# Performance work log

Measured on AMD Instinct MI355X. Metric: run time of the kernel, lower is better.

The kernel has to match this reference:

```python
import jax, jax.numpy as jnp
import numpy as np

D_MODEL = 1024
N_HEADS = 16
D_HEAD = D_MODEL // N_HEADS
WINDOW = 128
D_FF = 3 * D_MODEL
EPS = 1e-5


def _layer_norm(x, g, b):
    mu = jnp.mean(x, axis=-1, keepdims=True)
    var = jnp.var(x, axis=-1, keepdims=True)
    return (x - mu) * jax.lax.rsqrt(var + EPS) * g + b


def setup_inputs() -> dict:
    key = jax.random.key(0)
    ks = jax.random.split(key, 10)
    B, S = 2, 2048
    sd = 0.02
    return {
        "x": jax.random.normal(ks[0], (B, S, D_MODEL), dtype=jnp.float32),
        "w_qkv": jax.random.normal(ks[1], (D_MODEL, 3 * D_MODEL), dtype=jnp.float32) * sd,
        "b_qkv": jnp.zeros((3 * D_MODEL,), jnp.float32),
        "w_out": jax.random.normal(ks[2], (D_MODEL, D_MODEL), dtype=jnp.float32) * sd,
        "b_out": jnp.zeros((D_MODEL,), jnp.float32),
        "w_ff1": jax.random.normal(ks[3], (D_MODEL, D_FF), dtype=jnp.float32) * sd,
        "b_ff1": jnp.zeros((D_FF,), jnp.float32),
        "w_ff2": jax.random.normal(ks[4], (D_FF, D_MODEL), dtype=jnp.float32) * sd,
        "b_ff2": jnp.zeros((D_MODEL,), jnp.float32),
        "ln1_g": jnp.ones((D_MODEL,), jnp.float32),
        "ln1_b": jnp.zeros((D_MODEL,), jnp.float32),
        "ln2_g": jnp.ones((D_MODEL,), jnp.float32),
        "ln2_b": jnp.zeros((D_MODEL,), jnp.float32),
    }


def reference(x, w_qkv, b_qkv, w_out, b_out, w_ff1, b_ff1, w_ff2, b_ff2,
              ln1_g, ln1_b, ln2_g, ln2_b):
    B, S, D = x.shape
    h = _layer_norm(x, ln1_g, ln1_b)
    qkv = (h @ w_qkv + b_qkv).reshape(B, S, 3, N_HEADS, D_HEAD)
    q, k, v = (jnp.moveaxis(qkv[:, :, i], 1, 2) for i in range(3))  # (B,H,S,dh)
    scores = jnp.einsum('bhqd,bhkd->bhqk', q, k) / jnp.sqrt(jnp.float32(D_HEAD))
    i = jnp.arange(S)[:, None]
    j = jnp.arange(S)[None, :]
    allowed = (j <= i) & (j > i - WINDOW)  # causal sliding window band
    scores = jnp.where(allowed, scores, -jnp.inf)
    attn = jax.nn.softmax(scores, axis=-1)
    ctx = jnp.einsum('bhqk,bhkd->bqhd', attn, v).reshape(B, S, D)
    x = x + (ctx @ w_out + b_out)
    h2 = _layer_norm(x, ln2_g, ln2_b)
    ff = jax.nn.gelu(h2 @ w_ff1 + b_ff1, approximate=False) @ w_ff2 + b_ff2
    return x + ff
```

## Files before the change

kernel.cpp:

```cpp
#include <hip/hip_runtime.h>

#define D_MODEL 1024
#define SEQ 2048
#define BATCH 2
#define NH 16
#define DH 64
#define WIN 128
#define DFF 3072

typedef __bf16 bf16x8 __attribute__((ext_vector_type(8)));
typedef float f32x4 __attribute__((ext_vector_type(4)));
typedef unsigned short u16;
typedef unsigned int u32;

__device__ __forceinline__ float b2f(u16 u) {
    unsigned int x = ((unsigned int)u) << 16;
    return __uint_as_float(x);
}
__device__ __forceinline__ u16 f2b(float f) {
    unsigned int x = __float_as_uint(f);
    x += 0x7fffu + ((x >> 16) & 1u);
    return (u16)(x >> 16);
}
__device__ __forceinline__ u32 pk2(float a, float b) {
    return (u32)f2b(a) | ((u32)f2b(b) << 16);
}

#define WAIT_VMCNT0() __builtin_amdgcn_s_waitcnt(0x0F70)

__global__ __launch_bounds__(256) void prep_k(
        const float* __restrict__ x, const float* __restrict__ g1,
        const float* __restrict__ bt1, u16* __restrict__ hbf,
        const float* __restrict__ wqkv, u16* __restrict__ wqkvT,
        const float* __restrict__ wout, u16* __restrict__ woutT,
        const float* __restrict__ wff1, u16* __restrict__ wff1T,
        const float* __restrict__ wff2, u16* __restrict__ wff2T) {
    __shared__ u16 tile[32][33];
    __shared__ float s1[4], s2[4];
    int bid = blockIdx.x;
    if (bid < 10240) {
        const float* in; u16* out; int R, C, loc, gx;
        if (bid < 3072)      { in = wqkv; out = wqkvT; R = 1024; C = 3072; loc = bid;        gx = 96; }
        else if (bid < 4096) { in = wout; out = woutT; R = 1024; C = 1024; loc = bid - 3072; gx = 32; }
        else if (bid < 7168) { in = wff1; out = wff1T; R = 1024; C = 3072; loc = bid - 4096; gx = 96; }
        else                 { in = wff2; out = wff2T; R = 3072; C = 1024; loc = bid - 7168; gx = 32; }
        int bx = loc % gx, by = loc / gx;
        int tx = threadIdx.x & 31, ty = threadIdx.x >> 5;
        int r0 = by * 32, c0 = bx * 32;
#pragma unroll
        for (int i = 0; i < 4; ++i)
            tile[ty + i * 8][tx] = f2b(in[(size_t)(r0 + ty + i * 8) * C + c0 + tx]);
        __syncthreads();
#pragma unroll
        for (int i = 0; i < 4; ++i)
            out[(size_t)(c0 + ty + i * 8) * R + r0 + tx] = tile[tx][ty + i * 8];
    } else {
        int row = bid - 10240;
        const float* xr = x + (size_t)row * D_MODEL;
        float v[4];
        float sum = 0.f, sq = 0.f;
#pragma unroll
        for (int i = 0; i < 4; ++i) {
            v[i] = xr[threadIdx.x + i * 256];
            sum += v[i];
            sq += v[i] * v[i];
        }
#pragma unroll
        for (int off = 32; off > 0; off >>= 1) {
            sum += __shfl_xor(sum, off, 64);
            sq  += __shfl_xor(sq, off, 64);
        }
        int w = threadIdx.x >> 6;
        if ((threadIdx.x & 63) == 0) { s1[w] = sum; s2[w] = sq; }
        __syncthreads();
        sum = s1[0] + s1[1] + s1[2] + s1[3];
        sq  = s2[0] + s2[1] + s2[2] + s2[3];
        float mu = sum * (1.f / D_MODEL);
        float var = sq * (1.f / D_MODEL) - mu * mu;
        float rstd = rsqrtf(var + 1e-5f);
        u16* outr = hbf + (size_t)row * D_MODEL;
#pragma unroll
        for (int i = 0; i < 4; ++i) {
            int c = threadIdx.x + i * 256;
            outr[c] = f2b((v[i] - mu) * rstd * g1[c] + bt1[c]);
        }
    }
}

__global__ __launch_bounds__(256) void ln_k(
        const float* __restrict__ x, const float* __restrict__ g,
        const float* __restrict__ bta, u16* __restrict__ out) {
    int row = blockIdx.x;
    const float* xr = x + (size_t)row * D_MODEL;
    float v[4];
    float sum = 0.f, sq = 0.f;
#pragma unroll
    for (int i = 0; i < 4; ++i) {
        v[i] = xr[threadIdx.x + i * 256];
        sum += v[i];
        sq += v[i] * v[i];
    }
#pragma unroll
    for (int off = 32; off > 0; off >>= 1) {
        sum += __shfl_xor(sum, off, 64);
        sq  += __shfl_xor(sq, off, 64);
    }
    __shared__ float s1[4], s2[4];
    int w = threadIdx.x >> 6;
    if ((threadIdx.x & 63) == 0) { s1[w] = sum; s2[w] = sq; }
    __syncthreads();
    sum = s1[0] + s1[1] + s1[2] + s1[3];
    sq  = s2[0] + s2[1] + s2[2] + s2[3];
    float mu = sum * (1.f / D_MODEL);
    float var = sq * (1.f / D_MODEL) - mu * mu;
    float rstd = rsqrtf(var + 1e-5f);
    u16* outr = out + (size_t)row * D_MODEL;
#pragma unroll
    for (int i = 0; i < 4; ++i) {
        int c = threadIdx.x + i * 256;
        outr[c] = f2b((v[i] - mu) * rstd * g[c] + bta[c]);
    }
}

template <int GELU, int VSPLIT>
__global__ __launch_bounds__(256, 3) void gemm3_k(
        const u16* __restrict__ A, const u16* __restrict__ Bt,
        const float* __restrict__ bias, u16* __restrict__ Cb,
        u16* __restrict__ vt, int M, int N, int K, int ldc) {
    __shared__ u16 As[2 * 128 * 64];
    __shared__ u16 Bs[2 * 64 * 64];
    int tid = threadIdx.x;
    int w = tid >> 6, lane = tid & 63;
    int qd = lane >> 4, l15 = lane & 15;

    int lin = blockIdx.x;
    int xcd = lin & 7, idx = lin >> 3;
    int m0 = (xcd * 4 + (idx & 3)) * 128;
    int n0 = (idx >> 2) * 64;

    const u16* gsrc[6];
    u16* ldst[6];
    int nboff[6];
#pragma unroll
    for (int i = 0; i < 6; ++i) {
        int c = w * 6 + i;
        int isA = c < 16;
        int cb = isA ? c : c - 16;
        int row = cb * 8 + (lane >> 3);
        int cg = (lane & 7) ^ (row & 7);
        gsrc[i] = (isA ? A + (size_t)(m0 + row) * K
                       : Bt + (size_t)(n0 + row) * K) + cg * 8;
        ldst[i] = (isA ? As : Bs) + cb * 512;
        nboff[i] = isA ? 8192 : 4096;
    }

    int wm = w & 1, wn = w >> 1;
    f32x4 acc[4][2];
#pragma unroll
    for (int mt = 0; mt < 4; ++mt)
#pragma unroll
        for (int nt = 0; nt < 2; ++nt)
            acc[mt][nt] = (f32x4){0.f, 0.f, 0.f, 0.f};

    int aoff[4][2], boff[2][2];
#pragma unroll
    for (int t = 0; t < 4; ++t) {
        int ar = wm * 64 + t * 16 + l15;
#pragma unroll
        for (int h = 0; h < 2; ++h)
            aoff[t][h] = ar * 64 + (((h * 4 + qd) ^ (ar & 7)) * 8);
    }
#pragma unroll
    for (int t = 0; t < 2; ++t) {
        int br = wn * 32 + t * 16 + l15;
#pragma unroll
        for (int h = 0; h < 2; ++h)
            boff[t][h] = br * 64 + (((h * 4 + qd) ^ (br & 7)) * 8);
    }

#pragma unroll
    for (int i = 0; i < 6; ++i)
        __builtin_amdgcn_global_load_lds(
            (__attribute__((address_space(1))) void*)(gsrc[i]),
            (__attribute__((address_space(3))) void*)(ldst[i]), 16, 0, 0);

    int nsteps = K >> 6;

#define TSTEP3(S, RB)                                                       \
    {                                                                       \
        WAIT_VMCNT0();                                                      \
        __builtin_amdgcn_s_barrier();                                       \
        if ((S) + 1 < nsteps) {                                             \
            int k0 = ((S) + 1) << 6;                                        \
            _Pragma("unroll")                                               \
            for (int i = 0; i < 6; ++i)                                     \
                __builtin_amdgcn_global_load_lds(                           \
                    (__attribute__((address_space(1))) void*)(gsrc[i] + k0),\
                    (__attribute__((address_space(3))) void*)(ldst[i] +     \
                        (1 - (RB)) * nboff[i]),                             \
                    16, 0, 0);                                              \
        }                                                                   \
        bf16x8 av[4][2], bv[2][2];                                          \
        _Pragma("unroll")                                                   \
        for (int t = 0; t < 4; ++t)                                         \
            _Pragma("unroll")                                               \
            for (int h = 0; h < 2; ++h)                                     \
                av[t][h] = *(const bf16x8*)&As[aoff[t][h] + (RB) * 8192];   \
        _Pragma("unroll")                                                   \
        for (int t = 0; t < 2; ++t)                                         \
            _Pragma("unroll")                                               \
            for (int h = 0; h < 2; ++h)                                     \
                bv[t][h] = *(const bf16x8*)&Bs[boff[t][h] + (RB) * 4096];   \
        _Pragma("unroll")                                                   \
        for (int mt = 0; mt < 4; ++mt)                                      \
            _Pragma("unroll")                                               \
            for (int nt = 0; nt < 2; ++nt) {                                \
                acc[mt][nt] = __builtin_amdgcn_mfma_f32_16x16x32_bf16(      \
                    av[mt][0], bv[nt][0], acc[mt][nt], 0, 0, 0);            \
                acc[mt][nt] = __builtin_amdgcn_mfma_f32_16x16x32_bf16(      \
                    av[mt][1], bv[nt][1], acc[mt][nt], 0, 0, 0);            \
            }                                                               \
    }

    for (int s = 0; s < nsteps; s += 2) {
        TSTEP3(s, 0);
        TSTEP3(s + 1, 1);
    }

#pragma unroll
    for (int mt = 0; mt < 4; ++mt) {
        int row0 = m0 + wm * 64 + mt * 16 + qd * 4;
#pragma unroll
        for (int nt = 0; nt < 2; ++nt) {
            int col = n0 + wn * 32 + nt * 16 + l15;
            float v[4];
#pragma unroll
            for (int reg = 0; reg < 4; ++reg) {
                v[reg] = acc[mt][nt][reg] + bias[col];
                if (GELU) v[reg] = 0.5f * v[reg] * (1.f + erff(v[reg] * 0.70710678118654752f));
            }
            if (VSPLIT && col >= 2 * D_MODEL) {
                int d = col - 2 * D_MODEL;
                int bh = (row0 >> 11) * NH + (d >> 6);
                ushort4 pkv = {f2b(v[0]), f2b(v[1]), f2b(v[2]), f2b(v[3])};
                *(ushort4*)&vt[((size_t)(bh * DH + (d & 63))) * SEQ + (row0 & (SEQ - 1))] = pkv;
            } else {
#pragma unroll
                for (int reg = 0; reg < 4; ++reg)
                    Cb[(size_t)(row0 + reg) * ldc + col] = f2b(v[reg]);
            }
        }
    }
}

__global__ __launch_bounds__(256, 3) void gemm_tall_k(
        const u16* __restrict__ A, const u16* __restrict__ Bt,
        const float* __restrict__ bias, const float* __restrict__ resid,
        float* __restrict__ C, int M, int N, int K, int ldc) {
    __shared__ u16 As[2 * 64 * 64];
    __shared__ u16 Bs[2 * 128 * 64];
    int tid = threadIdx.x;
    int w = tid >> 6, lane = tid & 63;
    int qd = lane >> 4, l15 = lane & 15;

    int lin = blockIdx.x;
    int xcd = lin & 7, idx = lin >> 3;
    int m0 = (xcd * 8 + (idx & 7)) * 64;
    int n0 = (idx >> 3) * 128;

    const u16* gsrc[6];
    u16* ldst[6];
    int nboff[6];
#pragma unroll
    for (int i = 0; i < 6; ++i) {
        int c = w * 6 + i;
        int isA = c < 8;
        int cb = isA ? c : c - 8;
        int row = cb * 8 + (lane >> 3);
        int cg = (lane & 7) ^ (row & 7);
        gsrc[i] = (isA ? A + (size_t)(m0 + row) * K
                       : Bt + (size_t)(n0 + row) * K) + cg * 8;
        ldst[i] = (isA ? As : Bs) + cb * 512;
        nboff[i] = isA ? 4096 : 8192;
    }

    int wm = w & 1, wn = w >> 1;
    f32x4 acc[2][4];
#pragma unroll
    for (int mt = 0; mt < 2; ++mt)
#pragma unroll
        for (int nt = 0; nt < 4; ++nt)
            acc[mt][nt] = (f32x4){0.f, 0.f, 0.f, 0.f};

    int aoff[2][2], boff[4][2];
#pragma unroll
    for (int t = 0; t < 2; ++t) {
        int ar = wm * 32 + t * 16 + l15;
#pragma unroll
        for (int h = 0; h < 2; ++h)
            aoff[t][h] = ar * 64 + (((h * 4 + qd) ^ (ar & 7)) * 8);
    }
#pragma unroll
    for (int t = 0; t < 4; ++t) {
        int br = wn * 64 + t * 16 + l15;
#pragma unroll
        for (int h = 0; h < 2; ++h)
            boff[t][h] = br * 64 + (((h * 4 + qd) ^ (br & 7)) * 8);
    }

#pragma unroll
    for (int i = 0; i < 6; ++i)
        __builtin_amdgcn_global_load_lds(
            (__attribute__((address_space(1))) void*)(gsrc[i]),
            (__attribute__((address_space(3))) void*)(ldst[i]), 16, 0, 0);

    int nsteps = K >> 6;

#define TSTEP64(S, RB)                                                      \
    {                                                                       \
        WAIT_VMCNT0();                                                      \
        __builtin_amdgcn_s_barrier();                                       \
        if ((S) + 1 < nsteps) {                                             \
            int k0 = ((S) + 1) << 6;                                        \
            _Pragma("unroll")                                               \
            for (int i = 0; i < 6; ++i)                                     \
                __builtin_amdgcn_global_load_lds(                           \
                    (__attribute__((address_space(1))) void*)(gsrc[i] + k0),\
                    (__attribute__((address_space(3))) void*)(ldst[i] +     \
                        (1 - (RB)) * nboff[i]),                             \
                    16, 0, 0);                                              \
        }                                                                   \
        bf16x8 av[2][2], bv[4][2];                                          \
        _Pragma("unroll")                                                   \
        for (int t = 0; t < 2; ++t)                                         \
            _Pragma("unroll")                                               \
            for (int h = 0; h < 2; ++h)                                     \
                av[t][h] = *(const bf16x8*)&As[aoff[t][h] + (RB) * 4096];   \
        _Pragma("unroll")                                                   \
        for (int t = 0; t < 4; ++t)                                         \
            _Pragma("unroll")                                               \
            for (int h = 0; h < 2; ++h)                                     \
                bv[t][h] = *(const bf16x8*)&Bs[boff[t][h] + (RB) * 8192];   \
        _Pragma("unroll")                                                   \
        for (int mt = 0; mt < 2; ++mt)                                      \
            _Pragma("unroll")                                               \
            for (int nt = 0; nt < 4; ++nt) {                                \
                acc[mt][nt] = __builtin_amdgcn_mfma_f32_16x16x32_bf16(      \
                    av[mt][0], bv[nt][0], acc[mt][nt], 0, 0, 0);            \
                acc[mt][nt] = __builtin_amdgcn_mfma_f32_16x16x32_bf16(      \
                    av[mt][1], bv[nt][1], acc[mt][nt], 0, 0, 0);            \
            }                                                               \
    }

    for (int s = 0; s < nsteps; s += 2) {
        TSTEP64(s, 0);
        TSTEP64(s + 1, 1);
    }

#pragma unroll
    for (int mt = 0; mt < 2; ++mt) {
        int row0 = m0 + wm * 32 + mt * 16 + qd * 4;
#pragma unroll
        for (int nt = 0; nt < 4; ++nt) {
            int col = n0 + wn * 64 + nt * 16 + l15;
#pragma unroll
            for (int reg = 0; reg < 4; ++reg) {
                float v = acc[mt][nt][reg] + bias[col]
                        + resid[(size_t)(row0 + reg) * ldc + col];
                C[(size_t)(row0 + reg) * ldc + col] = v;
            }
        }
    }
}

__global__ __launch_bounds__(256) void attn_k(
        const u16* __restrict__ qk, const u16* __restrict__ vt,
        u16* __restrict__ ctx) {
    int lane = threadIdx.x & 63, l15 = lane & 15, quad = lane >> 4;
    int t = blockIdx.x * 4 + (threadIdx.x >> 6);
    int qt = t & (SEQ / 16 - 1);
    int h  = (t >> 7) & (NH - 1);
    int b  = t >> 11;
    int q0 = qt * 16;
    int bh = b * NH + h;

    const u16* qrow = qk + (size_t)(b * SEQ + q0 + l15) * (2 * D_MODEL) + h * DH + quad * 8;
    bf16x8 qf0 = *(const bf16x8*)(qrow);
    bf16x8 qf1 = *(const bf16x8*)(qrow + 32);
    const u16* kbase = qk + (size_t)(b * SEQ) * (2 * D_MODEL) + D_MODEL + h * DH + quad * 8;
    const u16* vbase = vt + (size_t)(bh * DH) * SEQ;

    f32x4 o[4] = {{0.f, 0.f, 0.f, 0.f}, {0.f, 0.f, 0.f, 0.f},
                  {0.f, 0.f, 0.f, 0.f}, {0.f, 0.f, 0.f, 0.f}};
    float m = -1e30f, l = 0.f;
    int q = q0 + l15;
    int cs = q0 - (WIN - 1);
    cs = cs < 0 ? 0 : (cs & ~31);

    for (int c = cs; c <= q0 + 15; c += 32) {
        const u16* k0p = kbase + (size_t)(c + l15) * (2 * D_MODEL);
        const u16* k1p = k0p + (size_t)16 * (2 * D_MODEL);
        bf16x8 ka0 = *(const bf16x8*)(k0p);
        bf16x8 ka1 = *(const bf16x8*)(k0p + 32);
        bf16x8 kb0 = *(const bf16x8*)(k1p);
        bf16x8 kb1 = *(const bf16x8*)(k1p + 32);
        f32x4 s0 = {0.f, 0.f, 0.f, 0.f}, s1 = {0.f, 0.f, 0.f, 0.f};
        s0 = __builtin_amdgcn_mfma_f32_16x16x32_bf16(ka0, qf0, s0, 0, 0, 0);
        s0 = __builtin_amdgcn_mfma_f32_16x16x32_bf16(ka1, qf1, s0, 0, 0, 0);
        s1 = __builtin_amdgcn_mfma_f32_16x16x32_bf16(kb0, qf0, s1, 0, 0, 0);
        s1 = __builtin_amdgcn_mfma_f32_16x16x32_bf16(kb1, qf1, s1, 0, 0, 0);

        float p0[4], p1[4];
        float cm = -1e30f;
#pragma unroll
        for (int reg = 0; reg < 4; ++reg) {
            int k0i = c + quad * 4 + reg;
            p0[reg] = ((unsigned)(q - k0i) < WIN) ? s0[reg] * 0.125f : -1e30f;
            p1[reg] = ((unsigned)(q - k0i - 16) < WIN) ? s1[reg] * 0.125f : -1e30f;
            cm = fmaxf(cm, fmaxf(p0[reg], p1[reg]));
        }
        cm = fmaxf(cm, __shfl_xor(cm, 16, 64));
        cm = fmaxf(cm, __shfl_xor(cm, 32, 64));
        float mn = fmaxf(m, cm);
        float alpha = __expf(m - mn);
        m = mn;
        float ls = 0.f;
#pragma unroll
        for (int reg = 0; reg < 4; ++reg) {
            p0[reg] = __expf(p0[reg] - mn);
            p1[reg] = __expf(p1[reg] - mn);
            ls += p0[reg] + p1[reg];
        }
        ls += __shfl_xor(ls, 16, 64);
        ls += __shfl_xor(ls, 32, 64);
        l = l * alpha + ls;
#pragma unroll
        for (int mt = 0; mt < 4; ++mt) o[mt] *= alpha;

        u32 z0 = pk2(p0[0], p0[1]), z1 = pk2(p0[2], p0[3]);
        u32 w0 = pk2(p1[0], p1[1]), w1 = pk2(p1[2], p1[3]);
        int slo = ((quad & 1) * 2) * 16 + l15;
        int shi = slo + 16;
        u32 zl0 = (u32)__shfl((int)z0, slo, 64), zl1 = (u32)__shfl((int)z1, slo, 64);
        u32 zh0 = (u32)__shfl((int)z0, shi, 64), zh1 = (u32)__shfl((int)z1, shi, 64);
        u32 wl0 = (u32)__shfl((int)w0, slo, 64), wl1 = (u32)__shfl((int)w1, slo, 64);
        u32 wh0 = (u32)__shfl((int)w0, shi, 64), wh1 = (u32)__shfl((int)w1, shi, 64);
        alignas(16) u32 pr[4];
        pr[0] = quad < 2 ? zl0 : wl0;
        pr[1] = quad < 2 ? zl1 : wl1;
        pr[2] = quad < 2 ? zh0 : wh0;
        pr[3] = quad < 2 ? zh1 : wh1;
        bf16x8 pf = *(const bf16x8*)pr;

#pragma unroll
        for (int mt = 0; mt < 4; ++mt) {
            bf16x8 vf = *(const bf16x8*)(vbase + (size_t)(mt * 16 + l15) * SEQ + c + quad * 8);
            o[mt] = __builtin_amdgcn_mfma_f32_16x16x32_bf16(vf, pf, o[mt], 0, 0, 0);
        }
    }

    float rdiv = 1.f / l;
    u16* crow = ctx + (size_t)(b * SEQ + q0 + l15) * D_MODEL + h * DH;
#pragma unroll
    for (int mt = 0; mt < 4; ++mt) {
        ushort4 pkv = {f2b(o[mt][0] * rdiv), f2b(o[mt][1] * rdiv),
                       f2b(o[mt][2] * rdiv), f2b(o[mt][3] * rdiv)};
        *(ushort4*)(crow + mt * 16 + quad * 4) = pkv;
    }
}

extern "C" void kernel_launch(void* const* d_in, const int* in_sizes, int n_in,
                              void* d_out, int out_size, void* d_ws, size_t ws_size,
                              hipStream_t stream) {
    (void)in_sizes; (void)n_in; (void)out_size; (void)ws_size;
    const float* x     = (const float*)d_in[0];
    const float* w_qkv = (const float*)d_in[1];
    const float* b_qkv = (const float*)d_in[2];
    const float* w_out = (const float*)d_in[3];
    const float* b_out = (const float*)d_in[4];
    const float* w_ff1 = (const float*)d_in[5];
    const float* b_ff1 = (const float*)d_in[6];
    const float* w_ff2 = (const float*)d_in[7];
    const float* b_ff2 = (const float*)d_in[8];
    const float* ln1g  = (const float*)d_in[9];
    const float* ln1b  = (const float*)d_in[10];
    const float* ln2g  = (const float*)d_in[11];
    const float* ln2b  = (const float*)d_in[12];
    float* out = (float*)d_out;

    const int M = BATCH * SEQ;
    char* base = (char*)d_ws;
    u16*   hbf   = (u16*)(base);
    u16*   qkbuf = (u16*)(base + (8ll  << 20));
    u16*   ctxbf = (u16*)(base + (24ll << 20));
    u16*   vtbuf = (u16*)(base + (32ll << 20));
    u16*   ffbf  = (u16*)(base + (8ll  << 20));
    float* x2    = (float*)(base + (40ll << 20));
    u16*   wqkvT = (u16*)(base + (56ll << 20));
    u16*   woutT = (u16*)(base + (62ll << 20));
    u16*   wff1T = (u16*)(base + (64ll << 20));
    u16*   wff2T = (u16*)(base + (70ll << 20));

    prep_k<<<dim3(14336), 256, 0, stream>>>(
        x, ln1g, ln1b, hbf, w_qkv, wqkvT, w_out, woutT,
        w_ff1, wff1T, w_ff2, wff2T);
    gemm3_k<0, 1><<<dim3((M / 128) * (3 * D_MODEL / 64)), 256, 0, stream>>>(
        hbf, wqkvT, b_qkv, qkbuf, vtbuf, M, 3 * D_MODEL, D_MODEL, 2 * D_MODEL);
    attn_k<<<dim3(BATCH * NH * (SEQ / 16) / 4), 256, 0, stream>>>(qkbuf, vtbuf, ctxbf);
    gemm_tall_k<<<dim3(512), 256, 0, stream>>>(
        ctxbf, woutT, b_out, x, x2, M, D_MODEL, D_MODEL, D_MODEL);
    ln_k<<<M, 256, 0, stream>>>(x2, ln2g, ln2b, hbf);
    gemm3_k<1, 0><<<dim3((M / 128) * (DFF / 64)), 256, 0, stream>>>(
        hbf, wff1T, b_ff1, ffbf, nullptr, M, DFF, D_MODEL, DFF);
    gemm_tall_k<<<dim3(512), 256, 0, stream>>>(
        ffbf, wff2T, b_ff2, x2, out, M, D_MODEL, DFF, D_MODEL);
}
```

Measured before the change: 273.1 us.

## Triple-buffer GEMM LDS tiles with two-stage-ahead async prefetch

Changes the GEMM main loop from double to triple buffering in LDS. Loads for step s+2 are issued while step s computes, and the wait uses a partial vmcnt so one stage of loads stays in flight. This is meant to hide global-to-LDS latency better. It costs more LDS per block (occupancy hint drops from 3 to 2 blocks per CU) and adds runtime buffer-index arithmetic in place of the unrolled two-step macro.

```diff
diff --git a/kernel.cpp b/kernel.cpp
--- a/kernel.cpp
+++ b/kernel.cpp
@@ -27,6 +27,7 @@
 }
 
 #define WAIT_VMCNT0() __builtin_amdgcn_s_waitcnt(0x0F70)
+#define WAIT_VMCNT6() __builtin_amdgcn_s_waitcnt(0x0F76)
 
 __global__ __launch_bounds__(256) void prep_k(
         const float* __restrict__ x, const float* __restrict__ g1,
@@ -123,12 +124,12 @@
 }
 
 template <int GELU, int VSPLIT>
-__global__ __launch_bounds__(256, 3) void gemm3_k(
+__global__ __launch_bounds__(256, 2) void gemm3_k(
         const u16* __restrict__ A, const u16* __restrict__ Bt,
         const float* __restrict__ bias, u16* __restrict__ Cb,
         u16* __restrict__ vt, int M, int N, int K, int ldc) {
-    __shared__ u16 As[2 * 128 * 64];
-    __shared__ u16 Bs[2 * 64 * 64];
+    __shared__ u16 As[3 * 128 * 64];
+    __shared__ u16 Bs[3 * 64 * 64];
     int tid = threadIdx.x;
     int w = tid >> 6, lane = tid & 63;
     int qd = lane >> 4, l15 = lane & 15;
@@ -140,7 +141,7 @@
 
     const u16* gsrc[6];
     u16* ldst[6];
-    int nboff[6];
+    int shr[6];
 #pragma unroll
     for (int i = 0; i < 6; ++i) {
         int c = w * 6 + i;
@@ -151,7 +152,7 @@
         gsrc[i] = (isA ? A + (size_t)(m0 + row) * K
                        : Bt + (size_t)(n0 + row) * K) + cg * 8;
         ldst[i] = (isA ? As : Bs) + cb * 512;
-        nboff[i] = isA ? 8192 : 4096;
+        shr[i] = isA ? 0 : 1;
     }
 
     int wm = w & 1, wn = w >> 1;
@@ -183,48 +184,53 @@
         __builtin_amdgcn_global_load_lds(
             (__attribute__((address_space(1))) void*)(gsrc[i]),
             (__attribute__((address_space(3))) void*)(ldst[i]), 16, 0, 0);
+#pragma unroll
+    for (int i = 0; i < 6; ++i)
+        __builtin_amdgcn_global_load_lds(
+            (__attribute__((address_space(1))) void*)(gsrc[i] + 64),
+            (__attribute__((address_space(3))) void*)(ldst[i] + (8192 >> shr[i])),
+            16, 0, 0);
 
     int nsteps = K >> 6;
-
-#define TSTEP3(S, RB)                                                       \
-    {                                                                       \
-        WAIT_VMCNT0();                                                      \
-        __builtin_amdgcn_s_barrier();                                       \
-        if ((S) + 1 < nsteps) {                                             \
-            int k0 = ((S) + 1) << 6;                                        \
-            _Pragma("unroll")                                               \
-            for (int i = 0; i < 6; ++i)                                     \
-                __builtin_amdgcn_global_load_lds(                           \
-                    (__attribute__((address_space(1))) void*)(gsrc[i] + k0),\
-                    (__attribute__((address_space(3))) void*)(ldst[i] +     \
-                        (1 - (RB)) * nboff[i]),                             \
-                    16, 0, 0);                                              \
-        }                                                                   \
-        bf16x8 av[4][2], bv[2][2];                                          \
-        _Pragma("unroll")                                                   \
-        for (int t = 0; t < 4; ++t)                                         \
-            _Pragma("unroll")                                               \
-            for (int h = 0; h < 2; ++h)                                     \
-                av[t][h] = *(const bf16x8*)&As[aoff[t][h] + (RB) * 8192];   \
-        _Pragma("unroll")                                                   \
-        for (int t = 0; t < 2; ++t)                                         \
-            _Pragma("unroll")                                               \
-            for (int h = 0; h < 2; ++h)                                     \
-                bv[t][h] = *(const bf16x8*)&Bs[boff[t][h] + (RB) * 4096];   \
-        _Pragma("unroll")                                                   \
-        for (int mt = 0; mt < 4; ++mt)                                      \
-            _Pragma("unroll")                                               \
-            for (int nt = 0; nt < 2; ++nt) {                                \
-                acc[mt][nt] = __builtin_amdgcn_mfma_f32_16x16x32_bf16(      \
-                    av[mt][0], bv[nt][0], acc[mt][nt], 0, 0, 0);            \
-                acc[mt][nt] = __builtin_amdgcn_mfma_f32_16x16x32_bf16(      \
-                    av[mt][1], bv[nt][1], acc[mt][nt], 0, 0, 0);            \
-            }                                                               \
-    }
-
-    for (int s = 0; s < nsteps; s += 2) {
-        TSTEP3(s, 0);
-        TSTEP3(s + 1, 1);
+    int curA = 0;
+    int pfA = 2 * 8192;
+
+    for (int s = 0; s < nsteps; ++s) {
+        if (s + 1 < nsteps) WAIT_VMCNT6();
+        else                WAIT_VMCNT0();
+        __builtin_amdgcn_s_barrier();
+        if (s + 2 < nsteps) {
+            int k0 = (s + 2) << 6;
+#pragma unroll
+            for (int i = 0; i < 6; ++i)
+                __builtin_amdgcn_global_load_lds(
+                    (__attribute__((address_space(1))) void*)(gsrc[i] + k0),
+                    (__attribute__((address_space(3))) void*)(ldst[i] + (pfA >> shr[i])),
+                    16, 0, 0);
+        }
+        int curB = curA >> 1;
+        bf16x8 av[4][2], bv[2][2];
+#pragma unroll
+        for (int t = 0; t < 4; ++t)
+#pragma unroll
+            for (int h = 0; h < 2; ++h)
+                av[t][h] = *(const bf16x8*)&As[aoff[t][h] + curA];
+#pragma unroll
+        for (int t = 0; t < 2; ++t)
+#pragma unroll
+            for (int h = 0; h < 2; ++h)
+                bv[t][h] = *(const bf16x8*)&Bs[boff[t][h] + curB];
+#pragma unroll
+        for (int mt = 0; mt < 4; ++mt)
+#pragma unroll
+            for (int nt = 0; nt < 2; ++nt) {
+                acc[mt][nt] = __builtin_amdgcn_mfma_f32_16x16x32_bf16(
+                    av[mt][0], bv[nt][0], acc[mt][nt], 0, 0, 0);
+                acc[mt][nt] = __builtin_amdgcn_mfma_f32_16x16x32_bf16(
+                    av[mt][1], bv[nt][1], acc[mt][nt], 0, 0, 0);
+            }
+        curA += 8192; if (curA == 3 * 8192) curA = 0;
+        pfA  += 8192; if (pfA  == 3 * 8192) pfA  = 0;
     }
 
 #pragma unroll
```

Measured after the change: 272.6 us. About the same (-0.2%).
